# Performance work log

Measured on AMD Instinct MI355X. Metric: run time of the kernel, lower is better.

Reference implementation:

```python
import jax, jax.numpy as jnp
import numpy as np

N, D, B, E, H = 512, 32, 4, 256, 4
SEP = 256
HD = E // H


def setup_inputs() -> dict:
    key = jax.random.key(0)
    ks = jax.random.split(key, 8)
    s = 0.02
    return {
        "src": jax.random.normal(ks[0], (N, D, B, E), dtype=jnp.float32),
        "w_in_row": jax.random.normal(ks[1], (3 * E, E), dtype=jnp.float32) * s,
        "b_in_row": jnp.zeros((3 * E,), jnp.float32),
        "w_out_row": jax.random.normal(ks[2], (E, E), dtype=jnp.float32) * s,
        "b_out_row": jnp.zeros((E,), jnp.float32),
        "w_in_col": jax.random.normal(ks[3], (3 * E, E), dtype=jnp.float32) * s,
        "b_in_col": jnp.zeros((3 * E,), jnp.float32),
        "w_out_col": jax.random.normal(ks[4], (E, E), dtype=jnp.float32) * s,
        "b_out_col": jnp.zeros((E,), jnp.float32),
        "ln_g": jnp.ones((E,), jnp.float32),
        "ln_b": jnp.zeros((E,), jnp.float32),
        "task_ids": jax.random.randint(ks[5], (B,), 0, 10),
        "single_eval_position": SEP,
    }


def _mha(x, w_in, b_in, w_out, b_out, mask):
    # x: (S, Bt, E); torch MultiheadAttention with batch_first=False
    S, Bt, _ = x.shape
    qkv = x @ w_in.T + b_in                      # (S, Bt, 3E)
    q, k, v = jnp.split(qkv, 3, axis=-1)
    to_heads = lambda t: t.reshape(S, Bt, H, HD).transpose(1, 2, 0, 3)  # (Bt,H,S,HD)
    q, k, v = to_heads(q), to_heads(k), to_heads(v)
    scores = jnp.einsum('bhqd,bhkd->bhqk', q, k) * (HD ** -0.5)
    if mask is not None:  # mask True == disallowed (torch convention)
        scores = jnp.where(mask[None, None], -jnp.inf, scores)
    attn = jax.nn.softmax(scores, axis=-1)
    out = jnp.einsum('bhqk,bhkd->bhqd', attn, v)
    out = out.transpose(2, 0, 1, 3).reshape(S, Bt, E)
    return out @ w_out.T + b_out


def _layer_norm(x, g, b, eps=1e-5):
    mu = x.mean(-1, keepdims=True)
    var = ((x - mu) ** 2).mean(-1, keepdims=True)
    return (x - mu) / jnp.sqrt(var + eps) * g + b


def reference(src, w_in_row, b_in_row, w_out_row, b_out_row,
              w_in_col, b_in_col, w_out_col, b_out_col,
              ln_g, ln_b, task_ids, single_eval_position):
    sep = single_eval_position
    idx = jnp.arange(N)
    # block mask: test queries may not attend to test keys
    row_mask = (idx[:, None] >= sep) & (idx[None, :] >= sep)
    # row attention over the N axis, batched across D*B
    src_row = _mha(src.reshape(N, D * B, E), w_in_row, b_in_row,
                   w_out_row, b_out_row, row_mask).reshape(N, D, B, E)
    # column attention over the D axis, batched across N*B (no mask)
    x_col = src.transpose(1, 0, 2, 3).reshape(D, N * B, E)
    src_col = _mha(x_col, w_in_col, b_in_col, w_out_col, b_out_col,
                   None).reshape(D, N, B, E).transpose(1, 0, 2, 3)
    # parallel axial (seq_axial=False), post-norm (pre_norm=False): row_norm unused
    return _layer_norm(src + src_row + src_col, ln_g, ln_b)
```

## Files before the change

### kernel.cpp

```cpp
#include <hip/hip_runtime.h>
#include <hip/hip_bf16.h>
#include <cstdint>
#include <cstddef>


typedef __hip_bfloat16 bf16;
typedef __attribute__((ext_vector_type(8))) short bf16x8;
typedef __attribute__((ext_vector_type(8))) short short8;
typedef __attribute__((ext_vector_type(4))) short bf16x4;
typedef __attribute__((ext_vector_type(4))) float f32x4;

#define NN 512
#define DD 32
#define BB 4
#define EE 256
#define HH 4
#define HDIM 64
#define DB (DD*BB)
#define MTOK (NN*DD*BB)
#define KBLK 64

__device__ __forceinline__ float bf2f(bf16 x){ return __bfloat162float(x); }
__device__ __forceinline__ short pkbf(float x){
  union { float f; uint32_t u; } c; c.f = x;
  return (short)((c.u + 0x8000u) >> 16);
}

#define AS1C(p) ((const __attribute__((address_space(1))) void*)(p))
#define AS3(p)  ((__attribute__((address_space(3))) void*)(p))

__global__ __launch_bounds__(256) void cvt_kernel(
    const float* __restrict__ in, bf16* __restrict__ out, int n)
{
  int i = (blockIdx.x * 256 + threadIdx.x) * 8;
  if (i >= n) return;
  const float* p = in + i;
  short8 o;
  #pragma unroll
  for (int j = 0; j < 8; ++j) ((short*)&o)[j] = pkbf(p[j]);
  *(short8*)(out + i) = o;
}

__global__ __launch_bounds__(256) void cvt_w_kernel(
    const float* __restrict__ ir, const float* __restrict__ ic,
    bf16* __restrict__ d_ir, bf16* __restrict__ d_ic)
{
  const int b = blockIdx.x;
  const float* src = (b < 96) ? ir : ic;
  bf16* dst = (b < 96) ? d_ir : d_ic;
  const int off = (b < 96) ? b : b - 96;
  const int i = (off * 256 + threadIdx.x) * 8;
  const float* p = src + i;
  short8 o;
  #pragma unroll
  for (int j = 0; j < 8; ++j) ((short*)&o)[j] = pkbf(p[j]);
  *(short8*)(dst + i) = o;
}

__global__ __launch_bounds__(256) void cvt_w2_kernel(
    const float* __restrict__ orr, const float* __restrict__ oc,
    bf16* __restrict__ d_or, bf16* __restrict__ d_oc)
{
  const int b = blockIdx.x;
  const float* src = (b < 32) ? orr : oc;
  bf16* dst = (b < 32) ? d_or : d_oc;
  const int off = (b < 32) ? b : b - 32;
  const int i = (off * 256 + threadIdx.x) * 8;
  const float* p = src + i;
  short8 o;
  #pragma unroll
  for (int j = 0; j < 8; ++j) ((short*)&o)[j] = pkbf(p[j]);
  *(short8*)(dst + i) = o;
}

template<int NT>
__global__ __launch_bounds__(256,2) void gemm_qkv(
    const bf16* __restrict__ A, const bf16* __restrict__ W1,
    const bf16* __restrict__ W2, const float* __restrict__ b1,
    const float* __restrict__ b2, bf16* __restrict__ C,
    const int nt1, const int nout)
{
  __shared__ bf16 As[128][64];
  __shared__ bf16 Bs[128][64];
  const int bid = blockIdx.x;
  const int xcd = bid & 7;
  const int i0  = bid >> 3;
  const int bm  = xcd * 64 + i0 / NT;
  const int bn  = i0 % NT;
  const int lbn = (bn < nt1) ? bn : bn - nt1;
  const bf16* W = (bn < nt1) ? W1 : W2;
  const float* bias = (bn < nt1) ? b1 : b2;

  const int tid  = threadIdx.x;
  const int wid  = tid >> 6;
  const int lane = tid & 63;
  const int lo = lane & 15, hi = lane >> 4;
  const int wr = wid >> 1, wc = wid & 1;

  const int srow = lane >> 3;
  const int ssrc = ((lane & 7) << 4) ^ (srow << 4);

  f32x4 acc[4][4] = {};

  for (int k0 = 0; k0 < 256; k0 += 64) {
    __syncthreads();
    #pragma unroll
    for (int i = 0; i < 4; ++i) {
      const int r = wid * 32 + i * 8 + srow;
      const int m = bm * 128 + r;
      const char* gpA = (const char*)(A + (size_t)m * EE + k0) + ssrc;
      __builtin_amdgcn_global_load_lds(AS1C(gpA), AS3(&As[wid*32 + i*8][0]), 16, 0, 0);
      const int wn = lbn * 128 + r;
      const char* gpB = (const char*)(W + (size_t)wn * EE + k0) + ssrc;
      __builtin_amdgcn_global_load_lds(AS1C(gpB), AS3(&Bs[wid*32 + i*8][0]), 16, 0, 0);
    }
    __syncthreads();

    #pragma unroll
    for (int kc = 0; kc < 2; ++kc) {
      const int cc = kc * 64 + hi * 16;
      bf16x8 af[4], bfr[4];
      #pragma unroll
      for (int i = 0; i < 4; ++i) {
        const int ra = wr * 64 + i * 16 + lo;
        af[i]  = *(const bf16x8*)((const char*)&As[ra][0] + (cc ^ ((ra & 7) << 4)));
        const int rb = wc * 64 + i * 16 + lo;
        bfr[i] = *(const bf16x8*)((const char*)&Bs[rb][0] + (cc ^ ((rb & 7) << 4)));
      }
      __builtin_amdgcn_s_setprio(1);
      #pragma unroll
      for (int mi = 0; mi < 4; ++mi)
        #pragma unroll
        for (int ni = 0; ni < 4; ++ni)
          acc[mi][ni] = __builtin_amdgcn_mfma_f32_16x16x32_bf16(
              af[mi], bfr[ni], acc[mi][ni], 0, 0, 0);
      __builtin_amdgcn_s_setprio(0);
    }
  }

  float bv[4];
  #pragma unroll
  for (int ni = 0; ni < 4; ++ni)
    bv[ni] = bias[lbn * 128 + wc * 64 + ni * 16 + lo];

  #pragma unroll
  for (int mi = 0; mi < 4; ++mi) {
    #pragma unroll
    for (int r = 0; r < 4; ++r) {
      const int m = bm * 128 + wr * 64 + mi * 16 + hi * 4 + r;
      #pragma unroll
      for (int ni = 0; ni < 4; ++ni) {
        const int col = bn * 128 + wc * 64 + ni * 16 + lo;
        C[(size_t)m * nout + col] = __hip_bfloat16_raw{(unsigned short)pkbf(acc[mi][ni][r] + bv[ni])};
      }
    }
  }
}

__global__ __launch_bounds__(256,2) void gemm_oproj(
    const bf16* __restrict__ A1, const bf16* __restrict__ A2,
    const bf16* __restrict__ W1, const bf16* __restrict__ W2,
    const float* __restrict__ b1, const float* __restrict__ b2,
    bf16* __restrict__ C1, bf16* __restrict__ C2)
{
  __shared__ bf16 As[128][64];
  __shared__ bf16 Bs[128][64];
  const int bid = blockIdx.x;
  const int sel = bid >> 10;
  const int b2i = bid & 1023;
  const int xcd = b2i & 7;
  const int i0  = b2i >> 3;
  const int bm  = xcd * 64 + (i0 >> 1);
  const int bn  = i0 & 1;
  const bf16* A = sel ? A2 : A1;
  const bf16* W = sel ? W2 : W1;
  const float* bias = sel ? b2 : b1;
  bf16* C = sel ? C2 : C1;

  const int tid  = threadIdx.x;
  const int wid  = tid >> 6;
  const int lane = tid & 63;
  const int lo = lane & 15, hi = lane >> 4;
  const int wr = wid >> 1, wc = wid & 1;

  const int srow = lane >> 3;
  const int ssrc = ((lane & 7) << 4) ^ (srow << 4);

  f32x4 acc[4][4] = {};

  for (int k0 = 0; k0 < 256; k0 += 64) {
    __syncthreads();
    #pragma unroll
    for (int i = 0; i < 4; ++i) {
      const int r = wid * 32 + i * 8 + srow;
      const int m = bm * 128 + r;
      const char* gpA = (const char*)(A + (size_t)m * EE + k0) + ssrc;
      __builtin_amdgcn_global_load_lds(AS1C(gpA), AS3(&As[wid*32 + i*8][0]), 16, 0, 0);
      const int wn = bn * 128 + r;
      const char* gpB = (const char*)(W + (size_t)wn * EE + k0) + ssrc;
      __builtin_amdgcn_global_load_lds(AS1C(gpB), AS3(&Bs[wid*32 + i*8][0]), 16, 0, 0);
    }
    __syncthreads();

    #pragma unroll
    for (int kc = 0; kc < 2; ++kc) {
      const int cc = kc * 64 + hi * 16;
      bf16x8 af[4], bfr[4];
      #pragma unroll
      for (int i = 0; i < 4; ++i) {
        const int ra = wr * 64 + i * 16 + lo;
        af[i]  = *(const bf16x8*)((const char*)&As[ra][0] + (cc ^ ((ra & 7) << 4)));
        const int rb = wc * 64 + i * 16 + lo;
        bfr[i] = *(const bf16x8*)((const char*)&Bs[rb][0] + (cc ^ ((rb & 7) << 4)));
      }
      __builtin_amdgcn_s_setprio(1);
      #pragma unroll
      for (int mi = 0; mi < 4; ++mi)
        #pragma unroll
        for (int ni = 0; ni < 4; ++ni)
          acc[mi][ni] = __builtin_amdgcn_mfma_f32_16x16x32_bf16(
              af[mi], bfr[ni], acc[mi][ni], 0, 0, 0);
      __builtin_amdgcn_s_setprio(0);
    }
  }

  float bv[4];
  #pragma unroll
  for (int ni = 0; ni < 4; ++ni)
    bv[ni] = bias[bn * 128 + wc * 64 + ni * 16 + lo];

  #pragma unroll
  for (int mi = 0; mi < 4; ++mi) {
    #pragma unroll
    for (int r = 0; r < 4; ++r) {
      const int m = bm * 128 + wr * 64 + mi * 16 + hi * 4 + r;
      #pragma unroll
      for (int ni = 0; ni < 4; ++ni) {
        const int col = bn * 128 + wc * 64 + ni * 16 + lo;
        C[(size_t)m * EE + col] = __hip_bfloat16_raw{(unsigned short)pkbf(acc[mi][ni][r] + bv[ni])};
      }
    }
  }
}

__global__ __launch_bounds__(256,4) void attn_axial(
    const bf16* __restrict__ baseR, const bf16* __restrict__ baseC,
    const int stride, bf16* __restrict__ attnR, bf16* __restrict__ attnC,
    const int* __restrict__ sep_ptr, const int nrow)
{
  __shared__ bf16 smem[9216];
  const int tid  = threadIdx.x;
  const int lane = tid & 63;
  const int lo = lane & 15, hi = lane >> 4;

  if ((int)blockIdx.x < nrow) {
    const int bid = blockIdx.x;
    const int xcd = bid & 7;
    const int idx = bid >> 3;
    const int pair = xcd * 64 + (idx >> 3);
    const int qt = idx & 7;
    const int t = pair >> 2;
    const int h = pair & 3;
    const int sep = *sep_ptr;
    const int wid = tid >> 6;
    bf16* Ks = smem;
    bf16* Vt = smem + 4608;

    const int qb = qt * 64;
    const int q0 = qb + wid * 16;

    bf16x8 qf[2];
    {
      const bf16* Qp = baseR + ((size_t)(q0 + lo) * DB + t) * stride + h * HDIM;
      bf16x8 a = *(const bf16x8*)(Qp + hi * 8);
      bf16x8 b = *(const bf16x8*)(Qp + 32 + hi * 8);
      #pragma unroll
      for (int j = 0; j < 8; ++j) {
        ((short*)&qf[0])[j] = pkbf(bf2f(((const bf16*)&a)[j]) * 0.125f);
        ((short*)&qf[1])[j] = pkbf(bf2f(((const bf16*)&b)[j]) * 0.125f);
      }
    }

    const int kr  = tid >> 2;
    const int kc4 = (tid & 3) * 16;
    const int vr  = tid & 63;
    const int vc  = (tid >> 6) * 16;
    const bf16* Kbase = baseR + ((size_t)kr * DB + t) * stride + EE + h * HDIM + kc4;
    const bf16* Vbase = baseR + ((size_t)vr * DB + t) * stride + 2*EE + h * HDIM + vc;
    const size_t kstep = (size_t)KBLK * DB * stride;

    f32x4 Oa[4] = {};
    float m_run = -1e30f, l_run = 0.f;

    const int nkt = (qb >= sep) ? ((sep + KBLK - 1) >> 6) : (NN >> 6);
    const bool need_mask = (qb + 64 > sep) && (nkt * KBLK > sep);

    bf16x8 kg0 = *(const bf16x8*)(Kbase);
    bf16x8 kg1 = *(const bf16x8*)(Kbase + 8);
    bf16x8 vg0 = *(const bf16x8*)(Vbase);
    bf16x8 vg1 = *(const bf16x8*)(Vbase + 8);

    for (int kt = 0; kt < nkt; ++kt) {
      const int k0 = kt * KBLK;

      *(bf16x8*)&Ks[kr*72 + kc4]     = kg0;
      *(bf16x8*)&Ks[kr*72 + kc4 + 8] = kg1;
      #pragma unroll
      for (int j = 0; j < 8; ++j) {
        Vt[(vc + j)*72 + vr]     = ((const bf16*)&vg0)[j];
        Vt[(vc + 8 + j)*72 + vr] = ((const bf16*)&vg1)[j];
      }
      __syncthreads();

      if (kt + 1 < nkt) {
        const size_t off = (size_t)(kt + 1) * kstep;
        kg0 = *(const bf16x8*)(Kbase + off);
        kg1 = *(const bf16x8*)(Kbase + off + 8);
        vg0 = *(const bf16x8*)(Vbase + off);
        vg1 = *(const bf16x8*)(Vbase + off + 8);
      }

      f32x4 st[4];
      {
        bf16x8 kf[4][2];
        #pragma unroll
        for (int kb = 0; kb < 4; ++kb)
          #pragma unroll
          for (int kc = 0; kc < 2; ++kc)
            kf[kb][kc] = *(const bf16x8*)&Ks[(kb*16 + lo)*72 + kc*32 + hi*8];
        __builtin_amdgcn_s_setprio(1);
        #pragma unroll
        for (int kb = 0; kb < 4; ++kb) {
          st[kb] = (f32x4){0,0,0,0};
          #pragma unroll
          for (int kc = 0; kc < 2; ++kc)
            st[kb] = __builtin_amdgcn_mfma_f32_16x16x32_bf16(
                kf[kb][kc], qf[kc], st[kb], 0, 0, 0);
        }
        __builtin_amdgcn_s_setprio(0);
      }

      if (need_mask && k0 + KBLK > sep) {
        const int qq = q0 + lo;
        #pragma unroll
        for (int kb = 0; kb < 4; ++kb)
          #pragma unroll
          for (int r = 0; r < 4; ++r) {
            const int kk = k0 + kb*16 + 4*hi + r;
            if (qq >= sep && kk >= sep) st[kb][r] = -1e30f;
          }
      }

      float mx = -1e30f;
      #pragma unroll
      for (int kb = 0; kb < 4; ++kb)
        #pragma unroll
        for (int r = 0; r < 4; ++r) mx = fmaxf(mx, st[kb][r]);
      mx = fmaxf(mx, __shfl_xor(mx, 16));
      mx = fmaxf(mx, __shfl_xor(mx, 32));

      if (__any(mx - m_run > 5.f)) {
        const float mn = fmaxf(m_run, mx);
        const float corr = __expf(m_run - mn);
        m_run = mn;
        l_run *= corr;
        float c4[4];
        #pragma unroll
        for (int r = 0; r < 4; ++r) c4[r] = __shfl(corr, hi*4 + r);
        #pragma unroll
        for (int n = 0; n < 4; ++n)
          #pragma unroll
          for (int r = 0; r < 4; ++r) Oa[n][r] *= c4[r];
      }

      float s0 = 0.f;
      #pragma unroll
      for (int kb = 0; kb < 4; ++kb)
        #pragma unroll
        for (int r = 0; r < 4; ++r) {
          const float pv = __expf(st[kb][r] - m_run);
          st[kb][r] = pv;
          s0 += pv;
        }
      s0 += __shfl_xor(s0, 16);
      s0 += __shfl_xor(s0, 32);
      l_run += s0;

      bf16x8 pa[2];
      #pragma unroll
      for (int kc = 0; kc < 2; ++kc)
        #pragma unroll
        for (int j = 0; j < 8; ++j)
          ((short*)&pa[kc])[j] = pkbf(st[kc*2 + (j>>2)][j&3]);

      __builtin_amdgcn_s_setprio(1);
      #pragma unroll
      for (int n = 0; n < 4; ++n) {
        #pragma unroll
        for (int kc = 0; kc < 2; ++kc) {
          const bf16* vrow = &Vt[(n*16 + lo)*72];
          bf16x4 v0 = *(const bf16x4*)(vrow + kc*32 + 4*hi);
          bf16x4 v1 = *(const bf16x4*)(vrow + kc*32 + 16 + 4*hi);
          bf16x8 vf = __builtin_shufflevector(v0, v1, 0,1,2,3,4,5,6,7);
          Oa[n] = __builtin_amdgcn_mfma_f32_16x16x32_bf16(pa[kc], vf, Oa[n], 0, 0, 0);
        }
      }
      __builtin_amdgcn_s_setprio(0);
      __syncthreads();
    }

    float linv[4];
    #pragma unroll
    for (int r = 0; r < 4; ++r) linv[r] = 1.f / __shfl(l_run, hi*4 + r);
    #pragma unroll
    for (int r = 0; r < 4; ++r) {
      const int qq = q0 + hi*4 + r;
      bf16* Op = attnR + ((size_t)qq * DB + t) * EE + h * HDIM;
      #pragma unroll
      for (int n = 0; n < 4; ++n)
        Op[n*16 + lo] = __hip_bfloat16_raw{(unsigned short)pkbf(Oa[n][r] * linv[r])};
    }
  } else {
    const int cb = blockIdx.x - nrow;
    const int n = cb >> 2;
    const int b = cb & 3;
    const int h = tid >> 6;

    {
      const int k  = tid & 31;
      const int hh = tid >> 6;
      const int dh = ((tid >> 5) & 1) * 32;
      const bf16* Vp = baseC + ((size_t)(n*DB + k*4 + b)) * stride + 2*EE + hh*64 + dh;
      #pragma unroll
      for (int c = 0; c < 4; ++c) {
        bf16x8 vv = *(const bf16x8*)(Vp + c*8);
        #pragma unroll
        for (int j = 0; j < 8; ++j)
          smem[hh*2304 + (dh + c*8 + j)*36 + k] = ((const bf16*)&vv)[j];
      }
    }

    bf16x8 qf[2][2], kf[2][2];
    #pragma unroll
    for (int mt = 0; mt < 2; ++mt) {
      const bf16* Qp = baseC + ((size_t)(n*DB + (mt*16 + lo)*4 + b)) * stride + h*64;
      #pragma unroll
      for (int kc = 0; kc < 2; ++kc) {
        bf16x8 v = *(const bf16x8*)(Qp + kc*32 + hi*8);
        #pragma unroll
        for (int j = 0; j < 8; ++j)
          ((short*)&v)[j] = pkbf(bf2f(((const bf16*)&v)[j]) * 0.125f);
        qf[mt][kc] = v;
      }
      const bf16* Kp = Qp + EE;
      kf[mt][0] = *(const bf16x8*)(Kp + hi*8);
      kf[mt][1] = *(const bf16x8*)(Kp + 32 + hi*8);
    }
    __syncthreads();

    f32x4 st[2][2];
    #pragma unroll
    for (int kt = 0; kt < 2; ++kt)
      #pragma unroll
      for (int mt = 0; mt < 2; ++mt) {
        f32x4 a = {0,0,0,0};
        a = __builtin_amdgcn_mfma_f32_16x16x32_bf16(kf[kt][0], qf[mt][0], a, 0, 0, 0);
        a = __builtin_amdgcn_mfma_f32_16x16x32_bf16(kf[kt][1], qf[mt][1], a, 0, 0, 0);
        st[kt][mt] = a;
      }

    float l[2];
    #pragma unroll
    for (int mt = 0; mt < 2; ++mt) {
      float mx = -1e30f;
      #pragma unroll
      for (int kt = 0; kt < 2; ++kt)
        #pragma unroll
        for (int r = 0; r < 4; ++r) mx = fmaxf(mx, st[kt][mt][r]);
      mx = fmaxf(mx, __shfl_xor(mx, 16));
      mx = fmaxf(mx, __shfl_xor(mx, 32));
      float s0 = 0.f;
      #pragma unroll
      for (int kt = 0; kt < 2; ++kt)
        #pragma unroll
        for (int r = 0; r < 4; ++r) {
          const float pv = __expf(st[kt][mt][r] - mx);
          st[kt][mt][r] = pv;
          s0 += pv;
        }
      s0 += __shfl_xor(s0, 16);
      s0 += __shfl_xor(s0, 32);
      l[mt] = s0;
    }

    bf16x8 pa[2];
    #pragma unroll
    for (int mt = 0; mt < 2; ++mt)
      #pragma unroll
      for (int j = 0; j < 8; ++j)
        ((short*)&pa[mt])[j] = pkbf(st[j>>2][mt][j&3]);

    f32x4 Oa[2][4] = {};
    #pragma unroll
    for (int nn = 0; nn < 4; ++nn) {
      const bf16* vrow = &smem[h*2304 + (nn*16 + lo)*36];
      bf16x4 v0 = *(const bf16x4*)(vrow + 4*hi);
      bf16x4 v1 = *(const bf16x4*)(vrow + 16 + 4*hi);
      bf16x8 vf = __builtin_shufflevector(v0, v1, 0,1,2,3,4,5,6,7);
      Oa[0][nn] = __builtin_amdgcn_mfma_f32_16x16x32_bf16(pa[0], vf, Oa[0][nn], 0, 0, 0);
      Oa[1][nn] = __builtin_amdgcn_mfma_f32_16x16x32_bf16(pa[1], vf, Oa[1][nn], 0, 0, 0);
    }

    float linv[2][4];
    #pragma unroll
    for (int mt = 0; mt < 2; ++mt)
      #pragma unroll
      for (int r = 0; r < 4; ++r)
        linv[mt][r] = 1.f / __shfl(l[mt], hi*4 + r);
    #pragma unroll
    for (int mt = 0; mt < 2; ++mt) {
      #pragma unroll
      for (int r = 0; r < 4; ++r) {
        const int q = mt*16 + hi*4 + r;
        bf16* Op = attnC + ((size_t)(n*DB + q*4 + b)) * EE + h*64;
        #pragma unroll
        for (int nn = 0; nn < 4; ++nn)
          Op[nn*16 + lo] = __hip_bfloat16_raw{(unsigned short)pkbf(Oa[mt][nn][r] * linv[mt][r])};
      }
    }
  }
}

__global__ __launch_bounds__(256) void ln_kernel(
    const float* __restrict__ src, const bf16* __restrict__ rp,
    const bf16* __restrict__ cp, const float* __restrict__ g,
    const float* __restrict__ b, float* __restrict__ out)
{
  const int m = blockIdx.x * 4 + (threadIdx.x >> 6);
  const int lane = threadIdx.x & 63;
  const float4 s4 = ((const float4*)src)[(size_t)m*64 + lane];
  const bf16x4 r4 = ((const bf16x4*)rp)[(size_t)m*64 + lane];
  const bf16x4 c4 = ((const bf16x4*)cp)[(size_t)m*64 + lane];
  float x[4];
  x[0] = s4.x + bf2f(((const bf16*)&r4)[0]) + bf2f(((const bf16*)&c4)[0]);
  x[1] = s4.y + bf2f(((const bf16*)&r4)[1]) + bf2f(((const bf16*)&c4)[1]);
  x[2] = s4.z + bf2f(((const bf16*)&r4)[2]) + bf2f(((const bf16*)&c4)[2]);
  x[3] = s4.w + bf2f(((const bf16*)&r4)[3]) + bf2f(((const bf16*)&c4)[3]);
  float sum = x[0] + x[1] + x[2] + x[3];
  #pragma unroll
  for (int off = 1; off < 64; off <<= 1) sum += __shfl_xor(sum, off);
  const float mu = sum * (1.f/EE);
  float d[4];
  #pragma unroll
  for (int j = 0; j < 4; ++j) d[j] = x[j] - mu;
  float ss = d[0]*d[0] + d[1]*d[1] + d[2]*d[2] + d[3]*d[3];
  #pragma unroll
  for (int off = 1; off < 64; off <<= 1) ss += __shfl_xor(ss, off);
  const float rstd = rsqrtf(ss * (1.f/EE) + 1e-5f);
  const float4 g4 = ((const float4*)g)[lane];
  const float4 b4 = ((const float4*)b)[lane];
  float4 o;
  o.x = d[0] * rstd * g4.x + b4.x;
  o.y = d[1] * rstd * g4.y + b4.y;
  o.z = d[2] * rstd * g4.z + b4.z;
  o.w = d[3] * rstd * g4.w + b4.w;
  ((float4*)out)[(size_t)m*64 + lane] = o;
}

extern "C" void kernel_launch(void* const* d_in, const int* in_sizes, int n_in,
                              void* d_out, int out_size, void* d_ws, size_t ws_size,
                              hipStream_t stream)
{
  const float* src      = (const float*)d_in[0];
  const float* w_in_row = (const float*)d_in[1];
  const float* b_in_row = (const float*)d_in[2];
  const float* w_out_row= (const float*)d_in[3];
  const float* b_out_row= (const float*)d_in[4];
  const float* w_in_col = (const float*)d_in[5];
  const float* b_in_col = (const float*)d_in[6];
  const float* w_out_col= (const float*)d_in[7];
  const float* b_out_col= (const float*)d_in[8];
  const float* ln_g     = (const float*)d_in[9];
  const float* ln_b     = (const float*)d_in[10];
  const int*   sep_ptr  = (const int*)d_in[12];
  float* out = (float*)d_out;

  char* ws = (char*)d_ws;
  dim3 blk(256);

  if (ws_size >= 268435456ULL) {
    bf16* qkv    = (bf16*)(ws);
    bf16* attnR  = (bf16*)(ws + 201326592);
    bf16* attnC  = (bf16*)(ws + 234881024);
    bf16* src_bf = attnR;
    bf16* wir    = (bf16*)(ws + 234881024);
    bf16* wic    = (bf16*)(ws + 235274240);
    bf16* wor    = (bf16*)(ws + 67108864);
    bf16* woc    = (bf16*)(ws + 67239936);
    bf16* r_out  = (bf16*)(ws);
    bf16* c_out  = (bf16*)(ws + 33554432);

    cvt_kernel<<<dim3(8192), blk, 0, stream>>>(src, src_bf, MTOK*EE);
    cvt_w_kernel<<<dim3(192), blk, 0, stream>>>(w_in_row, w_in_col, wir, wic);
    gemm_qkv<12><<<dim3(512*12), blk, 0, stream>>>(
        src_bf, wir, wic, b_in_row, b_in_col, qkv, 6, 1536);
    attn_axial<<<dim3(6144), blk, 0, stream>>>(
        qkv, qkv + 768, 1536, attnR, attnC, sep_ptr, 4096);
    cvt_w2_kernel<<<dim3(64), blk, 0, stream>>>(w_out_row, w_out_col, wor, woc);
    gemm_oproj<<<dim3(2048), blk, 0, stream>>>(
        attnR, attnC, wor, woc, b_out_row, b_out_col, r_out, c_out);
    ln_kernel<<<dim3(MTOK/4), blk, 0, stream>>>(src, r_out, c_out, ln_g, ln_b, out);
  } else {
    bf16* qkv    = (bf16*)(ws);
    bf16* attnR  = (bf16*)(ws + 100663296);
    bf16* attnC  = (bf16*)(ws + 134217728);
    bf16* src_bf = (bf16*)(ws + 167772160);
    bf16* wir    = (bf16*)(ws + 201326592);
    bf16* wic    = (bf16*)(ws + 201719808);
    bf16* wor    = (bf16*)(ws + 67108864);
    bf16* woc    = (bf16*)(ws + 67239936);
    bf16* r_out  = (bf16*)(ws);
    bf16* c_out  = (bf16*)(ws + 33554432);

    cvt_kernel<<<dim3(8192), blk, 0, stream>>>(src, src_bf, MTOK*EE);
    cvt_w_kernel<<<dim3(192), blk, 0, stream>>>(w_in_row, w_in_col, wir, wic);
    gemm_qkv<6><<<dim3(512*6), blk, 0, stream>>>(
        src_bf, wir, wir, b_in_row, b_in_row, qkv, 6, 768);
    attn_axial<<<dim3(4096), blk, 0, stream>>>(
        qkv, qkv, 768, attnR, attnC, sep_ptr, 4096);
    gemm_qkv<6><<<dim3(512*6), blk, 0, stream>>>(
        src_bf, wic, wic, b_in_col, b_in_col, qkv, 6, 768);
    attn_axial<<<dim3(2048), blk, 0, stream>>>(
        qkv, qkv, 768, attnR, attnC, sep_ptr, 0);
    cvt_w2_kernel<<<dim3(64), blk, 0, stream>>>(w_out_row, w_out_col, wor, woc);
    gemm_oproj<<<dim3(2048), blk, 0, stream>>>(
        attnR, attnC, wor, woc, b_out_row, b_out_col, r_out, c_out);
    ln_kernel<<<dim3(MTOK/4), blk, 0, stream>>>(src, r_out, c_out, ln_g, ln_b, out);
  }
}
```

Before: 257.0 us.

## Merge output projections into K-concatenated GEMM, widen attention blocks, use exp2

The row and column output projections become one GEMM over K=512 that writes a single summed tensor, so the layernorm reads one bf16 buffer instead of two. The source and weight conversion kernels are merged into one launch. The attention kernel moves to 512-thread blocks with 128-query tiles for row attention and two column units per block. Softmax uses exp2 with log2e folded into the query scale. The aim is less memory traffic, fewer launches and more K/V reuse, at the cost of larger LDS per block and possible occupancy changes.

Measured after the change: 447.8 us. 74.3% more time.

```diff
diff --git a/kernel.cpp b/kernel.cpp
--- a/kernel.cpp
+++ b/kernel.cpp
@@ -19,6 +19,9 @@
 #define DB (DD*BB)
 #define MTOK (NN*DD*BB)
 #define KBLK 64
+#define QSCALE 0.1803368801f
+
+extern "C" __device__ float __ocml_exp2_f32(float);
 
 __device__ __forceinline__ float bf2f(bf16 x){ return __bfloat162float(x); }
 __device__ __forceinline__ short pkbf(float x){
@@ -29,32 +32,22 @@
 #define AS1C(p) ((const __attribute__((address_space(1))) void*)(p))
 #define AS3(p)  ((__attribute__((address_space(3))) void*)(p))
 
-__global__ __launch_bounds__(256) void cvt_kernel(
-    const float* __restrict__ in, bf16* __restrict__ out, int n)
-{
-  int i = (blockIdx.x * 256 + threadIdx.x) * 8;
-  if (i >= n) return;
-  const float* p = in + i;
-  short8 o;
-  #pragma unroll
-  for (int j = 0; j < 8; ++j) ((short*)&o)[j] = pkbf(p[j]);
-  *(short8*)(out + i) = o;
-}
-
-__global__ __launch_bounds__(256) void cvt_w_kernel(
-    const float* __restrict__ ir, const float* __restrict__ ic,
-    bf16* __restrict__ d_ir, bf16* __restrict__ d_ic)
+__global__ __launch_bounds__(256) void cvt_main(
+    const float* __restrict__ src, const float* __restrict__ wirf,
+    const float* __restrict__ wicf, bf16* __restrict__ src_bf,
+    bf16* __restrict__ wir, bf16* __restrict__ wic)
 {
   const int b = blockIdx.x;
-  const float* src = (b < 96) ? ir : ic;
-  bf16* dst = (b < 96) ? d_ir : d_ic;
-  const int off = (b < 96) ? b : b - 96;
+  const float* s; bf16* d; int off;
+  if (b < 8192)      { s = src;  d = src_bf; off = b; }
+  else if (b < 8288) { s = wirf; d = wir;    off = b - 8192; }
+  else               { s = wicf; d = wic;    off = b - 8288; }
   const int i = (off * 256 + threadIdx.x) * 8;
-  const float* p = src + i;
+  const float* p = s + i;
   short8 o;
   #pragma unroll
   for (int j = 0; j < 8; ++j) ((short*)&o)[j] = pkbf(p[j]);
-  *(short8*)(dst + i) = o;
+  *(short8*)(d + i) = o;
 }
 
 __global__ __launch_bounds__(256) void cvt_w2_kernel(
@@ -161,21 +154,15 @@
     const bf16* __restrict__ A1, const bf16* __restrict__ A2,
     const bf16* __restrict__ W1, const bf16* __restrict__ W2,
     const float* __restrict__ b1, const float* __restrict__ b2,
-    bf16* __restrict__ C1, bf16* __restrict__ C2)
+    bf16* __restrict__ C)
 {
   __shared__ bf16 As[128][64];
   __shared__ bf16 Bs[128][64];
   const int bid = blockIdx.x;
-  const int sel = bid >> 10;
-  const int b2i = bid & 1023;
-  const int xcd = b2i & 7;
-  const int i0  = b2i >> 3;
+  const int xcd = bid & 7;
+  const int i0  = bid >> 3;
   const int bm  = xcd * 64 + (i0 >> 1);
   const int bn  = i0 & 1;
-  const bf16* A = sel ? A2 : A1;
-  const bf16* W = sel ? W2 : W1;
-  const float* bias = sel ? b2 : b1;
-  bf16* C = sel ? C2 : C1;
 
   const int tid  = threadIdx.x;
   const int wid  = tid >> 6;
@@ -188,16 +175,19 @@
 
   f32x4 acc[4][4] = {};
 
-  for (int k0 = 0; k0 < 256; k0 += 64) {
+  for (int k0 = 0; k0 < 512; k0 += 64) {
+    const bf16* A = (k0 < 256) ? A1 : A2;
+    const bf16* W = (k0 < 256) ? W1 : W2;
+    const int kk = k0 & 255;
     __syncthreads();
     #pragma unroll
     for (int i = 0; i < 4; ++i) {
       const int r = wid * 32 + i * 8 + srow;
       const int m = bm * 128 + r;
-      const char* gpA = (const char*)(A + (size_t)m * EE + k0) + ssrc;
+      const char* gpA = (const char*)(A + (size_t)m * EE + kk) + ssrc;
       __builtin_amdgcn_global_load_lds(AS1C(gpA), AS3(&As[wid*32 + i*8][0]), 16, 0, 0);
       const int wn = bn * 128 + r;
-      const char* gpB = (const char*)(W + (size_t)wn * EE + k0) + ssrc;
+      const char* gpB = (const char*)(W + (size_t)wn * EE + kk) + ssrc;
       __builtin_amdgcn_global_load_lds(AS1C(gpB), AS3(&Bs[wid*32 + i*8][0]), 16, 0, 0);
     }
     __syncthreads();
@@ -226,8 +216,10 @@
 
   float bv[4];
   #pragma unroll
-  for (int ni = 0; ni < 4; ++ni)
-    bv[ni] = bias[bn * 128 + wc * 64 + ni * 16 + lo];
+  for (int ni = 0; ni < 4; ++ni) {
+    const int col = bn * 128 + wc * 64 + ni * 16 + lo;
+    bv[ni] = b1[col] + b2[col];
+  }
 
   #pragma unroll
   for (int mi = 0; mi < 4; ++mi) {
@@ -243,30 +235,30 @@
   }
 }
 
-__global__ __launch_bounds__(256,4) void attn_axial(
+__global__ __launch_bounds__(512,8) void attn_axial(
     const bf16* __restrict__ baseR, const bf16* __restrict__ baseC,
     const int stride, bf16* __restrict__ attnR, bf16* __restrict__ attnC,
     const int* __restrict__ sep_ptr, const int nrow)
 {
-  __shared__ bf16 smem[9216];
+  __shared__ bf16 smem[18432];
   const int tid  = threadIdx.x;
-  const int lane = tid & 63;
-  const int lo = lane & 15, hi = lane >> 4;
 
   if ((int)blockIdx.x < nrow) {
     const int bid = blockIdx.x;
     const int xcd = bid & 7;
     const int idx = bid >> 3;
-    const int pair = xcd * 64 + (idx >> 3);
-    const int qt = idx & 7;
+    const int pair = xcd * 64 + (idx >> 2);
+    const int qt = idx & 3;
     const int t = pair >> 2;
     const int h = pair & 3;
     const int sep = *sep_ptr;
     const int wid = tid >> 6;
+    const int lane = tid & 63;
+    const int lo = lane & 15, hi = lane >> 4;
     bf16* Ks = smem;
     bf16* Vt = smem + 4608;
 
-    const int qb = qt * 64;
+    const int qb = qt * 128;
     const int q0 = qb + wid * 16;
 
     bf16x8 qf[2];
@@ -276,16 +268,16 @@
       bf16x8 b = *(const bf16x8*)(Qp + 32 + hi * 8);
       #pragma unroll
       for (int j = 0; j < 8; ++j) {
-        ((short*)&qf[0])[j] = pkbf(bf2f(((const bf16*)&a)[j]) * 0.125f);
-        ((short*)&qf[1])[j] = pkbf(bf2f(((const bf16*)&b)[j]) * 0.125f);
-      }
-    }
-
-    const int kr  = tid >> 2;
-    const int kc4 = (tid & 3) * 16;
+        ((short*)&qf[0])[j] = pkbf(bf2f(((const bf16*)&a)[j]) * QSCALE);
+        ((short*)&qf[1])[j] = pkbf(bf2f(((const bf16*)&b)[j]) * QSCALE);
+      }
+    }
+
+    const int kr  = tid >> 3;
+    const int kc8 = (tid & 7) * 8;
     const int vr  = tid & 63;
-    const int vc  = (tid >> 6) * 16;
-    const bf16* Kbase = baseR + ((size_t)kr * DB + t) * stride + EE + h * HDIM + kc4;
+    const int vc  = (tid >> 6) * 8;
+    const bf16* Kbase = baseR + ((size_t)kr * DB + t) * stride + EE + h * HDIM + kc8;
     const bf16* Vbase = baseR + ((size_t)vr * DB + t) * stride + 2*EE + h * HDIM + vc;
     const size_t kstep = (size_t)KBLK * DB * stride;
 
@@ -293,31 +285,24 @@
     float m_run = -1e30f, l_run = 0.f;
 
     const int nkt = (qb >= sep) ? ((sep + KBLK - 1) >> 6) : (NN >> 6);
-    const bool need_mask = (qb + 64 > sep) && (nkt * KBLK > sep);
-
-    bf16x8 kg0 = *(const bf16x8*)(Kbase);
-    bf16x8 kg1 = *(const bf16x8*)(Kbase + 8);
-    bf16x8 vg0 = *(const bf16x8*)(Vbase);
-    bf16x8 vg1 = *(const bf16x8*)(Vbase + 8);
+    const bool need_mask = (qb + 128 > sep) && (nkt * KBLK > sep);
+
+    bf16x8 kg = *(const bf16x8*)(Kbase);
+    bf16x8 vg = *(const bf16x8*)(Vbase);
 
     for (int kt = 0; kt < nkt; ++kt) {
       const int k0 = kt * KBLK;
 
-      *(bf16x8*)&Ks[kr*72 + kc4]     = kg0;
-      *(bf16x8*)&Ks[kr*72 + kc4 + 8] = kg1;
-      #pragma unroll
-      for (int j = 0; j < 8; ++j) {
-        Vt[(vc + j)*72 + vr]     = ((const bf16*)&vg0)[j];
-        Vt[(vc + 8 + j)*72 + vr] = ((const bf16*)&vg1)[j];
-      }
+      *(bf16x8*)&Ks[kr*72 + kc8] = kg;
+      #pragma unroll
+      for (int j = 0; j < 8; ++j)
+        Vt[(vc + j)*72 + vr] = ((const bf16*)&vg)[j];
       __syncthreads();
 
       if (kt + 1 < nkt) {
         const size_t off = (size_t)(kt + 1) * kstep;
-        kg0 = *(const bf16x8*)(Kbase + off);
-        kg1 = *(const bf16x8*)(Kbase + off + 8);
-        vg0 = *(const bf16x8*)(Vbase + off);
-        vg1 = *(const bf16x8*)(Vbase + off + 8);
+        kg = *(const bf16x8*)(Kbase + off);
+        vg = *(const bf16x8*)(Vbase + off);
       }
 
       f32x4 st[4];
@@ -361,7 +346,7 @@
 
       if (__any(mx - m_run > 5.f)) {
         const float mn = fmaxf(m_run, mx);
-        const float corr = __expf(m_run - mn);
+        const float corr = __ocml_exp2_f32(m_run - mn);
         m_run = mn;
         l_run *= corr;
         float c4[4];
@@ -378,7 +363,7 @@
       for (int kb = 0; kb < 4; ++kb)
         #pragma unroll
         for (int r = 0; r < 4; ++r) {
-          const float pv = __expf(st[kb][r] - m_run);
+          const float pv = __ocml_exp2_f32(st[kb][r] - m_run);
           st[kb][r] = pv;
           s0 += pv;
         }
@@ -421,22 +406,27 @@
         Op[n*16 + lo] = __hip_bfloat16_raw{(unsigned short)pkbf(Oa[n][r] * linv[r])};
     }
   } else {
-    const int cb = blockIdx.x - nrow;
+    const int unit = tid >> 8;
+    const int tl   = tid & 255;
+    const int cb = (blockIdx.x - nrow) * 2 + unit;
     const int n = cb >> 2;
     const int b = cb & 3;
-    const int h = tid >> 6;
+    const int h = tl >> 6;
+    const int lane = tl & 63;
+    const int lo = lane & 15, hi = lane >> 4;
+    bf16* sm = smem + unit * 9216;
 
     {
-      const int k  = tid & 31;
-      const int hh = tid >> 6;
-      const int dh = ((tid >> 5) & 1) * 32;
+      const int k  = tl & 31;
+      const int hh = tl >> 6;
+      const int dh = ((tl >> 5) & 1) * 32;
       const bf16* Vp = baseC + ((size_t)(n*DB + k*4 + b)) * stride + 2*EE + hh*64 + dh;
       #pragma unroll
       for (int c = 0; c < 4; ++c) {
         bf16x8 vv = *(const bf16x8*)(Vp + c*8);
         #pragma unroll
         for (int j = 0; j < 8; ++j)
-          smem[hh*2304 + (dh + c*8 + j)*36 + k] = ((const bf16*)&vv)[j];
+          sm[hh*2304 + (dh + c*8 + j)*36 + k] = ((const bf16*)&vv)[j];
       }
     }
 
@@ -449,7 +439,7 @@
         bf16x8 v = *(const bf16x8*)(Qp + kc*32 + hi*8);
         #pragma unroll
         for (int j = 0; j < 8; ++j)
-          ((short*)&v)[j] = pkbf(bf2f(((const bf16*)&v)[j]) * 0.125f);
+          ((short*)&v)[j] = pkbf(bf2f(((const bf16*)&v)[j]) * QSCALE);
         qf[mt][kc] = v;
       }
       const bf16* Kp = Qp + EE;
@@ -484,7 +474,7 @@
       for (int kt = 0; kt < 2; ++kt)
         #pragma unroll
         for (int r = 0; r < 4; ++r) {
-          const float pv = __expf(st[kt][mt][r] - mx);
+          const float pv = __ocml_exp2_f32(st[kt][mt][r] - mx);
           st[kt][mt][r] = pv;
           s0 += pv;
         }
@@ -503,7 +493,7 @@
     f32x4 Oa[2][4] = {};
     #pragma unroll
     for (int nn = 0; nn < 4; ++nn) {
-      const bf16* vrow = &smem[h*2304 + (nn*16 + lo)*36];
+      const bf16* vrow = &sm[h*2304 + (nn*16 + lo)*36];
       bf16x4 v0 = *(const bf16x4*)(vrow + 4*hi);
       bf16x4 v1 = *(const bf16x4*)(vrow + 16 + 4*hi);
       bf16x8 vf = __builtin_shufflevector(v0, v1, 0,1,2,3,4,5,6,7);
@@ -532,20 +522,19 @@
 }
 
 __global__ __launch_bounds__(256) void ln_kernel(
-    const float* __restrict__ src, const bf16* __restrict__ rp,
-    const bf16* __restrict__ cp, const float* __restrict__ g,
-    const float* __restrict__ b, float* __restrict__ out)
+    const float* __restrict__ src, const bf16* __restrict__ rc,
+    const float* __restrict__ g, const float* __restrict__ b,
+    float* __restrict__ out)
 {
   const int m = blockIdx.x * 4 + (threadIdx.x >> 6);
   const int lane = threadIdx.x & 63;
   const float4 s4 = ((const float4*)src)[(size_t)m*64 + lane];
-  const bf16x4 r4 = ((const bf16x4*)rp)[(size_t)m*64 + lane];
-  const bf16x4 c4 = ((const bf16x4*)cp)[(size_t)m*64 + lane];
+  const bf16x4 r4 = ((const bf16x4*)rc)[(size_t)m*64 + lane];
   float x[4];
-  x[0] = s4.x + bf2f(((const bf16*)&r4)[0]) + bf2f(((const bf16*)&c4)[0]);
-  x[1] = s4.y + bf2f(((const bf16*)&r4)[1]) + bf2f(((const bf16*)&c4)[1]);
-  x[2] = s4.z + bf2f(((const bf16*)&r4)[2]) + bf2f(((const bf16*)&c4)[2]);
-  x[3] = s4.w + bf2f(((const bf16*)&r4)[3]) + bf2f(((const bf16*)&c4)[3]);
+  x[0] = s4.x + bf2f(((const bf16*)&r4)[0]);
+  x[1] = s4.y + bf2f(((const bf16*)&r4)[1]);
+  x[2] = s4.z + bf2f(((const bf16*)&r4)[2]);
+  x[3] = s4.w + bf2f(((const bf16*)&r4)[3]);
   float sum = x[0] + x[1] + x[2] + x[3];
   #pragma unroll
   for (int off = 1; off < 64; off <<= 1) sum += __shfl_xor(sum, off);
@@ -586,7 +575,7 @@
   float* out = (float*)d_out;
 
   char* ws = (char*)d_ws;
-  dim3 blk(256);
+  dim3 blk(256), blk5(512);
 
   if (ws_size >= 268435456ULL) {
     bf16* qkv    = (bf16*)(ws);
@@ -597,19 +586,18 @@
     bf16* wic    = (bf16*)(ws + 235274240);
     bf16* wor    = (bf16*)(ws + 67108864);
     bf16* woc    = (bf16*)(ws + 67239936);
-    bf16* r_out  = (bf16*)(ws);
-    bf16* c_out  = (bf16*)(ws + 33554432);
-
-    cvt_kernel<<<dim3(8192), blk, 0, stream>>>(src, src_bf, MTOK*EE);
-    cvt_w_kernel<<<dim3(192), blk, 0, stream>>>(w_in_row, w_in_col, wir, wic);
+    bf16* rc     = (bf16*)(ws);
+
+    cvt_main<<<dim3(8384), blk, 0, stream>>>(src, w_in_row, w_in_col,
+                                             src_bf, wir, wic);
     gemm_qkv<12><<<dim3(512*12), blk, 0, stream>>>(
         src_bf, wir, wic, b_in_row, b_in_col, qkv, 6, 1536);
-    attn_axial<<<dim3(6144), blk, 0, stream>>>(
-        qkv, qkv + 768, 1536, attnR, attnC, sep_ptr, 4096);
+    attn_axial<<<dim3(3072), blk5, 0, stream>>>(
+        qkv, qkv + 768, 1536, attnR, attnC, sep_ptr, 2048);
     cvt_w2_kernel<<<dim3(64), blk, 0, stream>>>(w_out_row, w_out_col, wor, woc);
-    gemm_oproj<<<dim3(2048), blk, 0, stream>>>(
-        attnR, attnC, wor, woc, b_out_row, b_out_col, r_out, c_out);
-    ln_kernel<<<dim3(MTOK/4), blk, 0, stream>>>(src, r_out, c_out, ln_g, ln_b, out);
+    gemm_oproj<<<dim3(1024), blk, 0, stream>>>(
+        attnR, attnC, wor, woc, b_out_row, b_out_col, rc);
+    ln_kernel<<<dim3(MTOK/4), blk, 0, stream>>>(src, rc, ln_g, ln_b, out);
   } else {
     bf16* qkv    = (bf16*)(ws);
     bf16* attnR  = (bf16*)(ws + 100663296);
@@ -619,22 +607,21 @@
     bf16* wic    = (bf16*)(ws + 201719808);
     bf16* wor    = (bf16*)(ws + 67108864);
     bf16* woc    = (bf16*)(ws + 67239936);
-    bf16* r_out  = (bf16*)(ws);
-    bf16* c_out  = (bf16*)(ws + 33554432);
-
-    cvt_kernel<<<dim3(8192), blk, 0, stream>>>(src, src_bf, MTOK*EE);
-    cvt_w_kernel<<<dim3(192), blk, 0, stream>>>(w_in_row, w_in_col, wir, wic);
+    bf16* rc     = (bf16*)(ws);
+
+    cvt_main<<<dim3(8384), blk, 0, stream>>>(src, w_in_row, w_in_col,
+                                             src_bf, wir, wic);
     gemm_qkv<6><<<dim3(512*6), blk, 0, stream>>>(
         src_bf, wir, wir, b_in_row, b_in_row, qkv, 6, 768);
-    attn_axial<<<dim3(4096), blk, 0, stream>>>(
-        qkv, qkv, 768, attnR, attnC, sep_ptr, 4096);
+    attn_axial<<<dim3(2048), blk5, 0, stream>>>(
+        qkv, qkv, 768, attnR, attnC, sep_ptr, 2048);
     gemm_qkv<6><<<dim3(512*6), blk, 0, stream>>>(
         src_bf, wic, wic, b_in_col, b_in_col, qkv, 6, 768);
-    attn_axial<<<dim3(2048), blk, 0, stream>>>(
+    attn_axial<<<dim3(1024), blk5, 0, stream>>>(
         qkv, qkv, 768, attnR, attnC, sep_ptr, 0);
     cvt_w2_kernel<<<dim3(64), blk, 0, stream>>>(w_out_row, w_out_col, wor, woc);
-    gemm_oproj<<<dim3(2048), blk, 0, stream>>>(
-        attnR, attnC, wor, woc, b_out_row, b_out_col, r_out, c_out);
-    ln_kernel<<<dim3(MTOK/4), blk, 0, stream>>>(src, r_out, c_out, ln_g, ln_b, out);
+    gemm_oproj<<<dim3(1024), blk, 0, stream>>>(
+        attnR, attnC, wor, woc, b_out_row, b_out_col, rc);
+    ln_kernel<<<dim3(MTOK/4), blk, 0, stream>>>(src, rc, ln_g, ln_b, out);
   }
 }
```
